# Kernel tuning notes

Hardware: AMD Instinct MI355X
Metric: run time of the kernel (lower is better)

The kernel has to match this reference:

```python
import jax, jax.numpy as jnp
import numpy as np

T_MAX = 0.5
LN_EPS = 1e-5
B, N, D = 256, 16384, 512
NNZ = N * 33  # ~ (2*top_k+1) nonzeros per row of the sparse Laplacian
DF = 4 * D
DT = 32  # time-embedding hidden size


def _layernorm(x, g, b):
    mu = jnp.mean(x, axis=-1, keepdims=True)
    var = jnp.mean((x - mu) ** 2, axis=-1, keepdims=True)
    return (x - mu) * jax.lax.rsqrt(var + LN_EPS) * g + b


def setup_inputs() -> dict:
    key = jax.random.key(0)
    ks = jax.random.split(key, 16)

    def lin_w(k, fan_out, fan_in):
        return jax.random.normal(k, (fan_out, fan_in), jnp.float32) * (1.0 / np.sqrt(fan_in))

    inp = {}
    inp["x0"] = jax.random.uniform(ks[0], (B, N), jnp.float32)
    inp["t"] = jax.random.uniform(ks[1], (B,), jnp.float32)
    inp["L_vals"] = jax.random.normal(ks[2], (NNZ,), jnp.float32) * 0.1
    inp["W_in"] = lin_w(ks[3], D, N)
    inp["b_in"] = jnp.zeros((D,), jnp.float32)
    inp["W_out"] = lin_w(ks[4], N, D)
    inp["b_out"] = jnp.zeros((N,), jnp.float32)
    inp["W_qkv"] = lin_w(ks[5], 3 * D, D)
    inp["b_qkv"] = jnp.zeros((3 * D,), jnp.float32)
    inp["W_o"] = lin_w(ks[6], D, D)
    inp["b_o"] = jnp.zeros((D,), jnp.float32)
    inp["g1"] = jnp.ones((D,), jnp.float32)
    inp["be1"] = jnp.zeros((D,), jnp.float32)
    inp["g2"] = jnp.ones((D,), jnp.float32)
    inp["be2"] = jnp.zeros((D,), jnp.float32)
    inp["W_f1"] = lin_w(ks[7], DF, D)
    inp["b_f1"] = jnp.zeros((DF,), jnp.float32)
    inp["W_f2"] = lin_w(ks[8], D, DF)
    inp["b_f2"] = jnp.zeros((D,), jnp.float32)
    inp["W_t1"] = lin_w(ks[9], DT, 1)
    inp["b_t1"] = jnp.zeros((DT,), jnp.float32)
    inp["W_t2"] = lin_w(ks[10], D, DT)
    inp["b_t2"] = jnp.zeros((D,), jnp.float32)
    inp["L_rows"] = jax.random.randint(ks[11], (NNZ,), 0, N, jnp.int32)
    inp["L_cols"] = jax.random.randint(ks[12], (NNZ,), 0, N, jnp.int32)
    return inp


def reference(x0, t, L_vals, W_in, b_in, W_out, b_out, W_qkv, b_qkv, W_o, b_o,
              g1, be1, g2, be2, W_f1, b_f1, W_f2, b_f2, W_t1, b_t1, W_t2, b_t2,
              L_rows, L_cols):
    n_items = x0.shape[1]
    d_model = W_in.shape[0]
    t_cont = t * T_MAX  # per-sample diffusion time (explicit input, not RNG)

    # Batched sparse Laplacian diffusion (replaces the per-row torch.sparse.mm loop):
    # (L @ x.T)[i, b] = sum_e L_vals[e] * x0[b, L_cols[e]] aggregated to row L_rows[e]
    contrib = x0[:, L_cols] * L_vals                                  # (B, NNZ)
    Lx = jax.ops.segment_sum(contrib.T, L_rows, num_segments=n_items)  # (N, B)
    x_t = x0 - t_cont[:, None] * Lx.T                                  # (B, N)

    # Denoiser (eval mode: dropout off)
    h = x_t @ W_in.T + b_in                                            # (B, D)
    t_norm = t_cont / T_MAX
    te = jax.nn.silu(t_norm[:, None] @ W_t1.T + b_t1) @ W_t2.T + b_t2  # (B, D)
    h = h + te

    # MultiheadAttention on a length-1 sequence: softmax over one key is exactly 1,
    # so attn_out = out_proj(V) with V = h @ W_v.T + b_v.
    qkv = h @ W_qkv.T + b_qkv                                          # (B, 3D)
    v = qkv[:, 2 * d_model:]
    attn_out = v @ W_o.T + b_o

    h = _layernorm(h + attn_out, g1, be1)
    ff = jax.nn.gelu(h @ W_f1.T + b_f1, approximate=False) @ W_f2.T + b_f2
    h = _layernorm(h + ff, g2, be2)

    pred = h @ W_out.T + b_out                                         # (B, N)
    return jnp.mean((pred - x0) ** 2)
```

## Files before the change

kernel.cpp:

```cpp
#include <hip/hip_runtime.h>
#include <math.h>

#define Bb   256
#define Nn   16384
#define Dd   512
#define NNZn 540672
#define DFf  2048
#define SLOT 128

#define CVT_BLKS 2560
#define TR_BLKS  1024
#define BK_BLKS  2112

typedef __bf16 bf16;
typedef __bf16 bf16x4 __attribute__((ext_vector_type(4)));
typedef __bf16 bf16x8 __attribute__((ext_vector_type(8)));
typedef float  f32x4  __attribute__((ext_vector_type(4)));

__device__ __forceinline__ void gload16(const void* g, void* l) {
  __builtin_amdgcn_global_load_lds(
      (const __attribute__((address_space(1))) unsigned int*)g,
      (__attribute__((address_space(3))) unsigned int*)l, 16, 0, 0);
}

__global__ __launch_bounds__(256) void k_prep(
    const float* __restrict__ w_v, const float* __restrict__ w_o,
    const float* __restrict__ w_f1, const float* __restrict__ w_f2,
    bf16* __restrict__ o_v, bf16* __restrict__ o_o,
    bf16* __restrict__ o_f1, bf16* __restrict__ o_f2,
    const float* __restrict__ x0, bf16* __restrict__ x0T,
    const int* __restrict__ rows, const int* __restrict__ cols,
    const float* __restrict__ vals,
    int* __restrict__ counts, int2* __restrict__ ents) {
  __shared__ float tile[64][65];
  int blk = blockIdx.x;
  if (blk < CVT_BLKS) {
    int v = blk * 256 + threadIdx.x;
    const float* s; bf16* d; int base;
    if (v < 131072) {
      if (v < 65536) { s = w_v;  d = o_v;  base = 0; }
      else           { s = w_o;  d = o_o;  base = 65536; }
    } else {
      if (v < 393216) { s = w_f1; d = o_f1; base = 131072; }
      else            { s = w_f2; d = o_f2; base = 393216; }
    }
    int idx = (v - base) * 4;
    float4 x = *(const float4*)(s + idx);
    bf16x4 o;
    o[0] = (bf16)x.x; o[1] = (bf16)x.y; o[2] = (bf16)x.z; o[3] = (bf16)x.w;
    *(bf16x4*)(d + idx) = o;
  } else if (blk < CVT_BLKS + TR_BLKS) {
    int bx = blk - CVT_BLKS;
    int n0 = (bx & 255) * 64, b0 = (bx >> 8) * 64;
    int tx = threadIdx.x & 63, ty = threadIdx.x >> 6;
#pragma unroll
    for (int i = 0; i < 16; i++) {
      int bl = ty * 16 + i;
      tile[bl][tx] = x0[(size_t)(b0 + bl) * Nn + n0 + tx];
    }
    __syncthreads();
#pragma unroll
    for (int i = 0; i < 16; i++) {
      int nl = ty * 16 + i;
      x0T[(size_t)(n0 + nl) * Bb + b0 + tx] = (bf16)tile[tx][nl];
    }
  } else {
    int i = (blk - CVT_BLKS - TR_BLKS) * 256 + threadIdx.x;
    int r = rows[i];
    int p = atomicAdd(&counts[r], 1);
    if (p < SLOT)
      ents[(size_t)r * SLOT + p] = make_int2(cols[i], __float_as_int(vals[i]));
  }
}

__global__ __launch_bounds__(256) void k_lx(const bf16x4* __restrict__ x0T4,
                                            const int* __restrict__ counts,
                                            const int2* __restrict__ ents,
                                            bf16x4* __restrict__ Lx4) {
  int w = threadIdx.x >> 6, lane = threadIdx.x & 63;
  int r = blockIdx.x * 4 + w;
  __shared__ int2 esm[4][64];
  int cnt = counts[r];
  const int2* ep = ents + (size_t)r * SLOT;
  float a0 = 0.f, a1 = 0.f, a2 = 0.f, a3 = 0.f;
  float b0 = 0.f, b1 = 0.f, b2 = 0.f, b3 = 0.f;
  for (int base = 0; base < cnt; base += 64) {
    int m = cnt - base; if (m > 64) m = 64;
    if (lane < m) esm[w][lane] = ep[base + lane];
    int i = 0;
    for (; i + 1 < m; i += 2) {
      int2 e0 = esm[w][i], e1 = esm[w][i + 1];
      bf16x4 xv0 = x0T4[(size_t)e0.x * 64 + lane];
      bf16x4 xv1 = x0T4[(size_t)e1.x * 64 + lane];
      float v0 = __int_as_float(e0.y), v1 = __int_as_float(e1.y);
      a0 += v0 * (float)xv0[0]; a1 += v0 * (float)xv0[1];
      a2 += v0 * (float)xv0[2]; a3 += v0 * (float)xv0[3];
      b0 += v1 * (float)xv1[0]; b1 += v1 * (float)xv1[1];
      b2 += v1 * (float)xv1[2]; b3 += v1 * (float)xv1[3];
    }
    if (i < m) {
      int2 e0 = esm[w][i];
      bf16x4 xv0 = x0T4[(size_t)e0.x * 64 + lane];
      float v0 = __int_as_float(e0.y);
      a0 += v0 * (float)xv0[0]; a1 += v0 * (float)xv0[1];
      a2 += v0 * (float)xv0[2]; a3 += v0 * (float)xv0[3];
    }
  }
  bf16x4 o;
  o[0] = (bf16)(a0 + b0); o[1] = (bf16)(a1 + b1);
  o[2] = (bf16)(a2 + b2); o[3] = (bf16)(a3 + b3);
  Lx4[(size_t)r * 64 + lane] = o;
}

__global__ __launch_bounds__(256) void k_combine(const float* __restrict__ x0,
                                                 const bf16* __restrict__ Lx,
                                                 const float* __restrict__ t,
                                                 bf16* __restrict__ xt) {
  __shared__ float lxs[64][65];
  int n0 = blockIdx.x * 64, b0 = blockIdx.y * 64;
  int tx = threadIdx.x & 63, ty = threadIdx.x >> 6;
#pragma unroll
  for (int i = 0; i < 16; i++) {
    int nl = ty * 16 + i;
    lxs[nl][tx] = (float)Lx[(size_t)(n0 + nl) * Bb + b0 + tx];
  }
  __syncthreads();
#pragma unroll
  for (int i = 0; i < 16; i++) {
    int bl = ty * 16 + i;
    int b  = b0 + bl;
    float tc = t[b] * 0.5f;
    float v = x0[(size_t)b * Nn + n0 + tx] - tc * lxs[tx][bl];
    xt[(size_t)b * Nn + n0 + tx] = (bf16)v;
  }
}

template <int BM, int BN, int MODE, int ACT = 0, int BF32 = 0>
__global__ __launch_bounds__(256) void gemm_tn(
    const bf16* __restrict__ A, const void* __restrict__ Bmv,
    float* __restrict__ C, int N, int K, int kLen, int MN,
    const float* __restrict__ bias, const float* __restrict__ x0,
    float* __restrict__ lossOut) {
  constexpr int WM = BM / 2, WN = BN / 2, FM = WM / 16, FN = WN / 16;
  constexpr int PA = (BM * 64) / 4096, PB = (BN * 64) / 4096;
  __shared__ __align__(16) bf16 As[BM * 32];
  __shared__ __align__(16) bf16 Bs[BN * 32];
  const int tid = threadIdx.x;
  const int lane = tid & 63, w = tid >> 6;
  const int wm = w >> 1, wn = w & 1;
  const int mBase = blockIdx.x * BM, nBase = blockIdx.y * BN;
  const int k0 = blockIdx.z * kLen;

  f32x4 acc[FM][FN];
#pragma unroll
  for (int i = 0; i < FM; i++)
#pragma unroll
    for (int j = 0; j < FN; j++) acc[i][j] = {0.f, 0.f, 0.f, 0.f};

  for (int kk = 0; kk < kLen; kk += 32) {
    const int k = k0 + kk;
    __syncthreads();
#pragma unroll
    for (int p = 0; p < PA; p++) {
      int u = p * 256 + tid;
      gload16(A + (size_t)(mBase + (u >> 2)) * K + k + (u & 3) * 8,
              (char*)As + p * 4096 + w * 1024);
    }
    if constexpr (BF32) {
      const float* Bf = (const float*)Bmv;
#pragma unroll
      for (int p = 0; p < BN * 32 / 1024; p++) {
        int u = p * 256 + tid;
        int row = u >> 3, sub = u & 7;
        float4 x = *(const float4*)(Bf + (size_t)(nBase + row) * K + k + sub * 4);
        bf16x4 o;
        o[0] = (bf16)x.x; o[1] = (bf16)x.y; o[2] = (bf16)x.z; o[3] = (bf16)x.w;
        *(bf16x4*)(Bs + row * 32 + sub * 4) = o;
      }
    } else {
      const bf16* Bm = (const bf16*)Bmv;
#pragma unroll
      for (int p = 0; p < PB; p++) {
        int u = p * 256 + tid;
        gload16(Bm + (size_t)(nBase + (u >> 2)) * K + k + (u & 3) * 8,
                (char*)Bs + p * 4096 + w * 1024);
      }
    }
    __syncthreads();
    bf16x8 af[FM], bfr[FN];
#pragma unroll
    for (int i = 0; i < FM; i++)
      af[i] = *(const bf16x8*)(As + (wm * WM + i * 16 + (lane & 15)) * 32 + (lane >> 4) * 8);
#pragma unroll
    for (int j = 0; j < FN; j++)
      bfr[j] = *(const bf16x8*)(Bs + (wn * WN + j * 16 + (lane & 15)) * 32 + (lane >> 4) * 8);
#pragma unroll
    for (int i = 0; i < FM; i++)
#pragma unroll
      for (int j = 0; j < FN; j++)
        acc[i][j] = __builtin_amdgcn_mfma_f32_16x16x32_bf16(af[i], bfr[j], acc[i][j], 0, 0, 0);
  }

  if constexpr (MODE == 0) {
    float* Cz = C + (size_t)blockIdx.z * MN;
#pragma unroll
    for (int i = 0; i < FM; i++)
#pragma unroll
      for (int j = 0; j < FN; j++) {
        int n  = nBase + wn * WN + j * 16 + (lane & 15);
        int mB = mBase + wm * WM + i * 16 + ((lane >> 4) << 2);
#pragma unroll
        for (int r = 0; r < 4; r++)
          Cz[(size_t)(mB + r) * N + n] = acc[i][j][r];
      }
  } else if constexpr (MODE == 1) {
    bf16* Cb = (bf16*)C;
#pragma unroll
    for (int i = 0; i < FM; i++)
#pragma unroll
      for (int j = 0; j < FN; j++) {
        int n  = nBase + wn * WN + j * 16 + (lane & 15);
        float bo = bias[n];
        int mB = mBase + wm * WM + i * 16 + ((lane >> 4) << 2);
#pragma unroll
        for (int r = 0; r < 4; r++) {
          float x = acc[i][j][r] + bo;
          if constexpr (ACT == 1)
            x = 0.5f * x * (1.f + erff(x * 0.70710678118654752f));
          Cb[(size_t)(mB + r) * N + n] = (bf16)x;
        }
      }
  } else {
    float lsum = 0.f;
#pragma unroll
    for (int i = 0; i < FM; i++)
#pragma unroll
      for (int j = 0; j < FN; j++) {
        int n  = nBase + wn * WN + j * 16 + (lane & 15);
        float bo = bias[n];
        int mB = mBase + wm * WM + i * 16 + ((lane >> 4) << 2);
#pragma unroll
        for (int r = 0; r < 4; r++) {
          float d = acc[i][j][r] + bo - x0[(size_t)(mB + r) * N + n];
          lsum += d * d;
        }
      }
    for (int off = 32; off > 0; off >>= 1) lsum += __shfl_down(lsum, off, 64);
    if (lane == 0) atomicAdd(lossOut, lsum);
  }
}

__global__ __launch_bounds__(512) void k_epi_h(const float* __restrict__ P,
                                               const float* __restrict__ t,
                                               const float* __restrict__ W_t1,
                                               const float* __restrict__ b_t1,
                                               const float* __restrict__ W_t2,
                                               const float* __restrict__ b_t2,
                                               const float* __restrict__ b_in,
                                               float* __restrict__ h_f32,
                                               bf16* __restrict__ h_b) {
  int b = blockIdx.x, d = threadIdx.x;
  __shared__ float s[32];
  if (d < 32) {
    float z = t[b] * W_t1[d] + b_t1[d];
    s[d] = z / (1.f + expf(-z));
  }
  __syncthreads();
  int i = b * Dd + d;
  float v = b_in[d] + b_t2[d];
#pragma unroll
  for (int sp = 0; sp < 32; sp++) v += P[sp * (Bb * Dd) + i];
#pragma unroll
  for (int j = 0; j < 32; j++) v += s[j] * W_t2[d * 32 + j];
  h_f32[i] = v;
  h_b[i] = (bf16)v;
}

template <int NS>
__global__ __launch_bounds__(512) void k_ln(const float* __restrict__ base,
                                            const float* __restrict__ add,
                                            const float* __restrict__ bias,
                                            const float* __restrict__ g,
                                            const float* __restrict__ be,
                                            float* __restrict__ out_f32,
                                            bf16* __restrict__ out_b) {
  int b = blockIdx.x, d = threadIdx.x;
  __shared__ float red[16];
  int i = b * Dd + d;
  float x = base[i] + bias[d];
#pragma unroll
  for (int sp = 0; sp < NS; sp++) x += add[sp * (Bb * Dd) + i];
  int w = d >> 6, lane = d & 63;
  float s = x;
  for (int off = 32; off > 0; off >>= 1) s += __shfl_down(s, off, 64);
  if (lane == 0) red[w] = s;
  __syncthreads();
  if (d == 0) {
    float tot = 0.f;
    for (int q = 0; q < 8; q++) tot += red[q];
    red[8] = tot * (1.f / 512.f);
  }
  __syncthreads();
  float mu = red[8];
  float c = x - mu;
  float s2 = c * c;
  for (int off = 32; off > 0; off >>= 1) s2 += __shfl_down(s2, off, 64);
  if (lane == 0) red[w] = s2;
  __syncthreads();
  if (d == 0) {
    float tot = 0.f;
    for (int q = 0; q < 8; q++) tot += red[q];
    red[8] = tot * (1.f / 512.f);
  }
  __syncthreads();
  float var = red[8];
  float y = c * rsqrtf(var + 1e-5f) * g[d] + be[d];
  if (out_f32) out_f32[i] = y;
  out_b[i] = (bf16)y;
}

__global__ void k_final(const float* __restrict__ loss, float* __restrict__ out) {
  if (threadIdx.x == 0 && blockIdx.x == 0)
    out[0] = loss[0] * (1.f / 4194304.f);
}

extern "C" void kernel_launch(void* const* d_in, const int* in_sizes, int n_in,
                              void* d_out, int out_size, void* d_ws, size_t ws_size,
                              hipStream_t stream) {
  const float* x0    = (const float*)d_in[0];
  const float* t     = (const float*)d_in[1];
  const float* Lv    = (const float*)d_in[2];
  const float* W_in  = (const float*)d_in[3];
  const float* b_in  = (const float*)d_in[4];
  const float* W_out = (const float*)d_in[5];
  const float* b_out = (const float*)d_in[6];
  const float* W_qkv = (const float*)d_in[7];
  const float* b_qkv = (const float*)d_in[8];
  const float* W_o   = (const float*)d_in[9];
  const float* b_o   = (const float*)d_in[10];
  const float* g1    = (const float*)d_in[11];
  const float* be1   = (const float*)d_in[12];
  const float* g2    = (const float*)d_in[13];
  const float* be2   = (const float*)d_in[14];
  const float* W_f1  = (const float*)d_in[15];
  const float* b_f1  = (const float*)d_in[16];
  const float* W_f2  = (const float*)d_in[17];
  const float* b_f2  = (const float*)d_in[18];
  const float* W_t1  = (const float*)d_in[19];
  const float* b_t1  = (const float*)d_in[20];
  const float* W_t2  = (const float*)d_in[21];
  const float* b_t2  = (const float*)d_in[22];
  const int* L_rows  = (const int*)d_in[23];
  const int* L_cols  = (const int*)d_in[24];

  size_t off = 0;
  char* ws = (char*)d_ws;
  auto carve = [&](size_t bytes) -> void* {
    void* p = ws + off;
    off += (bytes + 255) & ~(size_t)255;
    return p;
  };

  bf16* W_v_b    = (bf16*)carve((size_t)Dd * Dd * 2);
  bf16* W_o_b    = (bf16*)carve((size_t)Dd * Dd * 2);
  bf16* W_f1_b   = (bf16*)carve((size_t)DFf * Dd * 2);
  bf16* W_f2_b   = (bf16*)carve((size_t)Dd * DFf * 2);
  bf16* x0T_b    = (bf16*)carve((size_t)Nn * Bb * 2);
  bf16* Lx_b     = (bf16*)carve((size_t)Nn * Bb * 2);
  bf16* xt_b     = (bf16*)carve((size_t)Bb * Nn * 2);
  float* p_h     = (float*)carve((size_t)32 * Bb * Dd * 4);
  float* p_at    = (float*)carve((size_t)Bb * Dd * 4);
  float* p_f2    = (float*)carve((size_t)4 * Bb * Dd * 4);
  float* h_f32   = (float*)carve((size_t)Bb * Dd * 4);
  bf16* h_b      = (bf16*)carve((size_t)Bb * Dd * 2);
  bf16* v_b      = (bf16*)carve((size_t)Bb * Dd * 2);
  float* hln_f32 = (float*)carve((size_t)Bb * Dd * 4);
  bf16* hln_b    = (bf16*)carve((size_t)Bb * Dd * 2);
  bf16* f1_b     = (bf16*)carve((size_t)Bb * DFf * 2);
  bf16* h2_b     = (bf16*)carve((size_t)Bb * Dd * 2);
  int* counts    = (int*)carve((size_t)Nn * 4);
  float* lossw   = (float*)carve(256);
  int2* ents     = (int2*)carve((size_t)Nn * SLOT * 8);
  (void)in_sizes; (void)n_in; (void)out_size; (void)ws_size; (void)Lv;

  hipMemsetAsync(counts, 0, (size_t)Nn * 4 + 256, stream);

  k_prep<<<CVT_BLKS + TR_BLKS + BK_BLKS, 256, 0, stream>>>(
      W_qkv + (size_t)2 * Dd * Dd, W_o, W_f1, W_f2,
      W_v_b, W_o_b, W_f1_b, W_f2_b,
      x0, x0T_b, L_rows, L_cols, Lv, counts, ents);

  k_lx<<<Nn / 4, 256, 0, stream>>>((const bf16x4*)x0T_b, counts, ents,
                                   (bf16x4*)Lx_b);
  k_combine<<<dim3(256, 4), 256, 0, stream>>>(x0, Lx_b, t, xt_b);

  gemm_tn<128, 128, 0, 0, 1><<<dim3(2, 4, 32), 256, 0, stream>>>(
      xt_b, W_in, p_h, Dd, Nn, 512, Bb * Dd, nullptr, nullptr, nullptr);
  k_epi_h<<<Bb, 512, 0, stream>>>(p_h, t, W_t1, b_t1, W_t2, b_t2, b_in, h_f32, h_b);

  gemm_tn<64, 64, 1><<<dim3(4, 8, 1), 256, 0, stream>>>(
      h_b, W_v_b, (float*)v_b, Dd, Dd, 512, 0, b_qkv + 2 * Dd, nullptr, nullptr);

  gemm_tn<64, 64, 0><<<dim3(4, 8, 1), 256, 0, stream>>>(
      v_b, W_o_b, p_at, Dd, Dd, 512, 0, nullptr, nullptr, nullptr);
  k_ln<1><<<Bb, 512, 0, stream>>>(h_f32, p_at, b_o, g1, be1, hln_f32, hln_b);

  gemm_tn<64, 64, 1, 1><<<dim3(4, 32, 1), 256, 0, stream>>>(
      hln_b, W_f1_b, (float*)f1_b, DFf, Dd, 512, 0, b_f1, nullptr, nullptr);

  gemm_tn<64, 64, 0><<<dim3(4, 8, 4), 256, 0, stream>>>(
      f1_b, W_f2_b, p_f2, Dd, DFf, 512, Bb * Dd, nullptr, nullptr, nullptr);
  k_ln<4><<<Bb, 512, 0, stream>>>(hln_f32, p_f2, b_f2, g2, be2, nullptr, h2_b);

  gemm_tn<128, 128, 2, 0, 1><<<dim3(2, 128, 1), 256, 0, stream>>>(
      h2_b, W_out, nullptr, Nn, Dd, 512, 0, b_out, x0, lossw);
  k_final<<<1, 64, 0, stream>>>(lossw, (float*)d_out);
}
```

Baseline: 330.9 us.

## Double-buffer GEMM K-loop with register-staged fp32 B and retune split-K tiles

Converts the GEMM main loop to double-buffered LDS. The next A tile is issued asynchronously, and the next fp32 B tile is prefetched into registers and converted to bf16 after the current MFMAs, so there is one barrier per iteration instead of two. The W_in GEMM moves to 64x64 tiles with split-K of 16 and kLen 1024, and its epilogue reduction is adjusted to match. The output GEMM moves to 64x128 tiles for more blocks, and the loss reduction now does one atomic per block instead of one per wave. LDS use doubles and more registers are held, which may lower occupancy; smaller tiles also re-read W_in and W_out more often.

```diff
diff --git a/kernel.cpp b/kernel.cpp
--- a/kernel.cpp
+++ b/kernel.cpp
@@ -142,14 +142,19 @@
     const float* __restrict__ bias, const float* __restrict__ x0,
     float* __restrict__ lossOut) {
   constexpr int WM = BM / 2, WN = BN / 2, FM = WM / 16, FN = WN / 16;
-  constexpr int PA = (BM * 64) / 4096, PB = (BN * 64) / 4096;
-  __shared__ __align__(16) bf16 As[BM * 32];
-  __shared__ __align__(16) bf16 Bs[BN * 32];
+  constexpr int PA  = (BM * 64) / 4096;
+  constexpr int PB  = (BN * 64) / 4096;
+  constexpr int PBV = BN / 32;
+  constexpr int NB  = BF32 ? PBV : 1;
+  __shared__ __align__(16) bf16 As[2][BM * 32];
+  __shared__ __align__(16) bf16 Bs[2][BN * 32];
+  __shared__ float lred[4];
   const int tid = threadIdx.x;
   const int lane = tid & 63, w = tid >> 6;
   const int wm = w >> 1, wn = w & 1;
   const int mBase = blockIdx.x * BM, nBase = blockIdx.y * BN;
   const int k0 = blockIdx.z * kLen;
+  const int nIter = kLen >> 5;
 
   f32x4 acc[FM][FN];
 #pragma unroll
@@ -157,48 +162,75 @@
 #pragma unroll
     for (int j = 0; j < FN; j++) acc[i][j] = {0.f, 0.f, 0.f, 0.f};
 
-  for (int kk = 0; kk < kLen; kk += 32) {
-    const int k = k0 + kk;
-    __syncthreads();
+  float4 breg[NB];
+
+  auto stageA = [&](int buf, int k) {
 #pragma unroll
     for (int p = 0; p < PA; p++) {
       int u = p * 256 + tid;
       gload16(A + (size_t)(mBase + (u >> 2)) * K + k + (u & 3) * 8,
-              (char*)As + p * 4096 + w * 1024);
-    }
-    if constexpr (BF32) {
-      const float* Bf = (const float*)Bmv;
-#pragma unroll
-      for (int p = 0; p < BN * 32 / 1024; p++) {
-        int u = p * 256 + tid;
-        int row = u >> 3, sub = u & 7;
-        float4 x = *(const float4*)(Bf + (size_t)(nBase + row) * K + k + sub * 4);
-        bf16x4 o;
-        o[0] = (bf16)x.x; o[1] = (bf16)x.y; o[2] = (bf16)x.z; o[3] = (bf16)x.w;
-        *(bf16x4*)(Bs + row * 32 + sub * 4) = o;
-      }
-    } else {
-      const bf16* Bm = (const bf16*)Bmv;
-#pragma unroll
-      for (int p = 0; p < PB; p++) {
-        int u = p * 256 + tid;
-        gload16(Bm + (size_t)(nBase + (u >> 2)) * K + k + (u & 3) * 8,
-                (char*)Bs + p * 4096 + w * 1024);
-      }
-    }
+              (char*)As[buf] + p * 4096 + w * 1024);
+    }
+  };
+  auto stageBg = [&](int buf, int k) {
+    const bf16* Bm = (const bf16*)Bmv;
+#pragma unroll
+    for (int p = 0; p < PB; p++) {
+      int u = p * 256 + tid;
+      gload16(Bm + (size_t)(nBase + (u >> 2)) * K + k + (u & 3) * 8,
+              (char*)Bs[buf] + p * 4096 + w * 1024);
+    }
+  };
+  auto loadBreg = [&](int k) {
+    const float* Bf = (const float*)Bmv;
+#pragma unroll
+    for (int p = 0; p < NB; p++) {
+      int u = p * 256 + tid;
+      int row = u >> 3, sub = u & 7;
+      breg[p] = *(const float4*)(Bf + (size_t)(nBase + row) * K + k + sub * 4);
+    }
+  };
+  auto storeBreg = [&](int buf) {
+#pragma unroll
+    for (int p = 0; p < NB; p++) {
+      int u = p * 256 + tid;
+      int row = u >> 3, sub = u & 7;
+      bf16x4 o;
+      o[0] = (bf16)breg[p].x; o[1] = (bf16)breg[p].y;
+      o[2] = (bf16)breg[p].z; o[3] = (bf16)breg[p].w;
+      *(bf16x4*)(Bs[buf] + row * 32 + sub * 4) = o;
+    }
+  };
+
+  stageA(0, k0);
+  if constexpr (BF32) { loadBreg(k0); storeBreg(0); }
+  else stageBg(0, k0);
+  __syncthreads();
+
+  for (int t = 0; t < nIter; t++) {
+    const int cur = t & 1;
+    const bool more = (t + 1 < nIter);
+    if (more) {
+      stageA(cur ^ 1, k0 + (t + 1) * 32);
+      if constexpr (BF32) loadBreg(k0 + (t + 1) * 32);
+      else stageBg(cur ^ 1, k0 + (t + 1) * 32);
+    }
+    {
+      bf16x8 af[FM], bfr[FN];
+#pragma unroll
+      for (int i = 0; i < FM; i++)
+        af[i] = *(const bf16x8*)(As[cur] + (wm * WM + i * 16 + (lane & 15)) * 32 + (lane >> 4) * 8);
+#pragma unroll
+      for (int j = 0; j < FN; j++)
+        bfr[j] = *(const bf16x8*)(Bs[cur] + (wn * WN + j * 16 + (lane & 15)) * 32 + (lane >> 4) * 8);
+#pragma unroll
+      for (int i = 0; i < FM; i++)
+#pragma unroll
+        for (int j = 0; j < FN; j++)
+          acc[i][j] = __builtin_amdgcn_mfma_f32_16x16x32_bf16(af[i], bfr[j], acc[i][j], 0, 0, 0);
+    }
+    if constexpr (BF32) { if (more) storeBreg(cur ^ 1); }
     __syncthreads();
-    bf16x8 af[FM], bfr[FN];
-#pragma unroll
-    for (int i = 0; i < FM; i++)
-      af[i] = *(const bf16x8*)(As + (wm * WM + i * 16 + (lane & 15)) * 32 + (lane >> 4) * 8);
-#pragma unroll
-    for (int j = 0; j < FN; j++)
-      bfr[j] = *(const bf16x8*)(Bs + (wn * WN + j * 16 + (lane & 15)) * 32 + (lane >> 4) * 8);
-#pragma unroll
-    for (int i = 0; i < FM; i++)
-#pragma unroll
-      for (int j = 0; j < FN; j++)
-        acc[i][j] = __builtin_amdgcn_mfma_f32_16x16x32_bf16(af[i], bfr[j], acc[i][j], 0, 0, 0);
   }
 
   if constexpr (MODE == 0) {
@@ -246,7 +278,10 @@
         }
       }
     for (int off = 32; off > 0; off >>= 1) lsum += __shfl_down(lsum, off, 64);
-    if (lane == 0) atomicAdd(lossOut, lsum);
+    if (lane == 0) lred[w] = lsum;
+    __syncthreads();
+    if (tid == 0)
+      atomicAdd(lossOut, lred[0] + lred[1] + lred[2] + lred[3]);
   }
 }
 
@@ -269,7 +304,7 @@
   int i = b * Dd + d;
   float v = b_in[d] + b_t2[d];
 #pragma unroll
-  for (int sp = 0; sp < 32; sp++) v += P[sp * (Bb * Dd) + i];
+  for (int sp = 0; sp < 16; sp++) v += P[sp * (Bb * Dd) + i];
 #pragma unroll
   for (int j = 0; j < 32; j++) v += s[j] * W_t2[d * 32 + j];
   h_f32[i] = v;
@@ -394,8 +429,8 @@
                                    (bf16x4*)Lx_b);
   k_combine<<<dim3(256, 4), 256, 0, stream>>>(x0, Lx_b, t, xt_b);
 
-  gemm_tn<128, 128, 0, 0, 1><<<dim3(2, 4, 32), 256, 0, stream>>>(
-      xt_b, W_in, p_h, Dd, Nn, 512, Bb * Dd, nullptr, nullptr, nullptr);
+  gemm_tn<64, 64, 0, 0, 1><<<dim3(4, 8, 16), 256, 0, stream>>>(
+      xt_b, W_in, p_h, Dd, Nn, 1024, Bb * Dd, nullptr, nullptr, nullptr);
   k_epi_h<<<Bb, 512, 0, stream>>>(p_h, t, W_t1, b_t1, W_t2, b_t2, b_in, h_f32, h_b);
 
   gemm_tn<64, 64, 1><<<dim3(4, 8, 1), 256, 0, stream>>>(
@@ -412,7 +447,7 @@
       f1_b, W_f2_b, p_f2, Dd, DFf, 512, Bb * Dd, nullptr, nullptr, nullptr);
   k_ln<4><<<Bb, 512, 0, stream>>>(hln_f32, p_f2, b_f2, g2, be2, nullptr, h2_b);
 
-  gemm_tn<128, 128, 2, 0, 1><<<dim3(2, 128, 1), 256, 0, stream>>>(
+  gemm_tn<64, 128, 2, 0, 1><<<dim3(4, 128, 1), 256, 0, stream>>>(
       h2_b, W_out, nullptr, Nn, Dd, 512, 0, b_out, x0, lossw);
   k_final<<<1, 64, 0, stream>>>(lossw, (float*)d_out);
 }
```

After: 320.5 us. -3.1%, faster.
